# Performance work log

Measured on AMD Instinct MI355X. Metric: run time of the kernel, lower is better.

## Reference

```python
import jax, jax.numpy as jnp
import numpy as np

EPS_SCALE = 1e-4

def setup_inputs() -> dict:
    key = jax.random.key(0)
    B, D, K = 4096, 64, 256
    x = jax.random.normal(key, (B, D, K), dtype=jnp.float32)
    return {"x": x}

def reference(x):
    # x: [B, D, K]  (batch, cluster_dim, num_clusters) -- training path
    B, D, K = x.shape
    mu = jnp.mean(x, axis=0, keepdims=True)              # [1, D, K]
    xc = jnp.transpose(x - mu, (2, 1, 0))                # [K, D, B]
    cov = jnp.einsum('kdb,keb->kde', xc, xc) / (B - 1)   # [K, D, D]
    eps = EPS_SCALE * jnp.eye(D, dtype=x.dtype)
    L = jnp.linalg.cholesky(cov + eps)                   # [K, D, D]
    Z = jax.scipy.linalg.solve_triangular(L, xc, lower=True)  # [K, D, B]
    return jnp.transpose(Z, (2, 1, 0))                   # [B, D, K]
```

## Files before the change

### kernel.cpp

```cpp
#include <hip/hip_runtime.h>
#include <math.h>

#define Bn 4096
#define Dn 64
#define Kn 256
#define DKn 16384
#define SLAB ((size_t)262144)

typedef __attribute__((ext_vector_type(8))) short bf16x8;
typedef __attribute__((ext_vector_type(4))) float f32x4;
typedef unsigned short u16;
typedef unsigned int u32;

__device__ __forceinline__ float bf2f(u16 u) {
  return __uint_as_float(((u32)u) << 16);
}
__device__ __forceinline__ u16 f2bf(float f) {
  u32 x = __float_as_uint(f);
  u32 r = x + 0x7fffu + ((x >> 16) & 1u);
  return (u16)(r >> 16);
}

__global__ __launch_bounds__(256) void k1_transpose(
    const float* __restrict__ x, u16* __restrict__ xh) {
  __shared__ __align__(16) u16 tile[64][72];
  const int b0 = blockIdx.x * 8;
  const int k0 = blockIdx.y * 64;
  const int t = threadIdx.x;
  const int kq = t & 15, dsub = t >> 4;
  const int kr = t >> 3, dq = t & 7;

  for (int bb = 0; bb < 8; ++bb) {
    const int b = b0 + bb;
#pragma unroll
    for (int i = 0; i < 4; ++i) {
      const int d = dsub + 16 * i;
      const float4 v = *(const float4*)&x[(size_t)b * DKn + (size_t)d * Kn + k0 + 4 * kq];
      tile[4 * kq + 0][d] = f2bf(v.x);
      tile[4 * kq + 1][d] = f2bf(v.y);
      tile[4 * kq + 2][d] = f2bf(v.z);
      tile[4 * kq + 3][d] = f2bf(v.w);
    }
    __syncthreads();
#pragma unroll
    for (int it = 0; it < 2; ++it) {
      const int k = kr + 32 * it;
      const uint4 wv = *(const uint4*)&tile[k][8 * dq];
      *(uint4*)&xh[(size_t)(k0 + k) * SLAB + (size_t)b * 64 + 8 * dq] = wv;
    }
    __syncthreads();
  }
}

__global__ __launch_bounds__(256) void k2_cov(
    const u16* __restrict__ xh, float* __restrict__ covp, float* __restrict__ Sp) {
  __shared__ __align__(16) u16 tile[64][136];
  __shared__ float sred[32][64];
  const int part = blockIdx.x;
  const int k = blockIdx.y;
  const int t = threadIdx.x;
  const int w = t >> 6, l = t & 63;
  const int r16 = l & 15, g = l >> 4;
  const int dw = t & 7, bq = t >> 3;
  const u16* pk = xh + (size_t)k * SLAB;

  f32x4 hh[10];
#pragma unroll
  for (int p = 0; p < 10; ++p) hh[p] = (f32x4){0.f, 0.f, 0.f, 0.f};
  float sums[8];
#pragma unroll
  for (int jj = 0; jj < 8; ++jj) sums[jj] = 0.f;

  for (int sub = 0; sub < 8; ++sub) {
    const int bbase = part * 1024 + sub * 128;
    __syncthreads();
#pragma unroll
    for (int i = 0; i < 4; ++i) {
      const int b = bq * 4 + i;
      const uint4 v = *(const uint4*)&pk[(size_t)(bbase + b) * 64 + dw * 8];
      const u16* pv = (const u16*)&v;
#pragma unroll
      for (int jj = 0; jj < 8; ++jj) {
        const u16 h = pv[jj];
        sums[jj] += bf2f(h);
        tile[dw * 8 + jj][b] = h;
      }
    }
    __syncthreads();
    bf16x8 fr[4];
#pragma unroll
    for (int m = 0; m < 4; ++m)
      fr[m] = *(const bf16x8*)&tile[16 * m + r16][32 * w + 8 * g];
#pragma unroll
    for (int m = 0; m < 4; ++m)
#pragma unroll
      for (int n = m; n < 4; ++n) {
        const int p = (m * (7 - m)) / 2 + n;
        hh[p] = __builtin_amdgcn_mfma_f32_16x16x32_bf16(fr[m], fr[n], hh[p], 0, 0, 0);
      }
  }
  float* cp = covp + ((size_t)k * 16 + part * 4 + w) * 2560;
#pragma unroll
  for (int p = 0; p < 10; ++p)
#pragma unroll
    for (int r = 0; r < 4; ++r)
      cp[p * 256 + (g * 4 + r) * 16 + r16] = hh[p][r];
#pragma unroll
  for (int jj = 0; jj < 8; ++jj) sred[bq][dw * 8 + jj] = sums[jj];
  __syncthreads();
  if (t < 64) {
    float s = 0.f;
#pragma unroll
    for (int q = 0; q < 32; ++q) s += sred[q][t];
    Sp[((size_t)k * 4 + part) * 64 + t] = s;
  }
}

__global__ __launch_bounds__(256) void k3_chol(
    const float* __restrict__ covp, const float* __restrict__ Sp,
    u16* __restrict__ wt, u16* __restrict__ vout) {
  __shared__ float a[64][65];
  __shared__ float mus[64];
  __shared__ float colv[64];
  __shared__ float diag;
  const int k = blockIdx.x;
  const int tid = threadIdx.x;
  if (tid < 64) {
    float s = 0.f;
#pragma unroll
    for (int q = 0; q < 4; ++q) s += Sp[((size_t)k * 4 + q) * 64 + tid];
    mus[tid] = s * (1.f / 4096.f);
  }
  __syncthreads();
  const float* cp = covp + (size_t)k * 16 * 2560;
  for (int idx = tid; idx < 4096; idx += 256) {
    const int i = idx >> 6, j = idx & 63;
    const int i16 = i >> 4, j16 = j >> 4, r = i & 15, c = j & 15;
    int p, off;
    if (i16 <= j16) { p = (i16 * (7 - i16)) / 2 + j16; off = r * 16 + c; }
    else            { p = (j16 * (7 - j16)) / 2 + i16; off = c * 16 + r; }
    float s = 0.f;
#pragma unroll
    for (int q = 0; q < 16; ++q) s += cp[q * 2560 + p * 256 + off];
    float cv = (s - 4096.f * mus[i] * mus[j]) * (1.f / 4095.f);
    if (i == j) cv += 1e-4f;
    a[i][j] = cv;
  }
  __syncthreads();
  for (int j = 0; j < 64; ++j) {
    if (tid == j) diag = sqrtf(a[j][j]);
    __syncthreads();
    const float ljj = diag;
    float lij = 0.f;
    if (tid == j) a[j][j] = ljj;
    if (tid < 64 && tid > j) {
      lij = a[tid][j] / ljj;
      a[tid][j] = lij;
      colv[tid] = lij;
    }
    __syncthreads();
    if (tid < 64 && tid > j)
      for (int e = j + 1; e <= tid; ++e) a[tid][e] -= lij * colv[e];
    __syncthreads();
  }
  float wv[64];
  if (tid < 64) {
#pragma unroll
    for (int i = 0; i < 64; ++i) {
      float s2 = (i == tid) ? 1.f : 0.f;
#pragma unroll
      for (int j = 0; j < i; ++j) s2 -= a[i][j] * wv[j];
      wv[i] = (i >= tid) ? s2 / a[i][i] : 0.f;
    }
  }
  __syncthreads();
  if (tid < 64) {
#pragma unroll
    for (int i = 0; i < 64; ++i) a[i][tid] = wv[i];
  }
  __syncthreads();
  if (tid < 64) {
    float v = 0.f;
#pragma unroll
    for (int e = 0; e < 64; ++e) v += a[tid][e] * mus[e];
    vout[(size_t)k * 64 + tid] = f2bf(v);
  }
#pragma unroll
  for (int it = 0; it < 8; ++it) {
    const int idx = it * 256 + tid;
    const int dd = idx >> 5, ep = idx & 31;
    const u32 pk2 = (u32)f2bf(a[dd][2 * ep]) | ((u32)f2bf(a[dd][2 * ep + 1]) << 16);
    *(u32*)&wt[(size_t)k * 4096 + 2 * idx] = pk2;
  }
}

__global__ __launch_bounds__(256) void k45_solve(
    const u16* __restrict__ xh, const u16* __restrict__ wt,
    const u16* __restrict__ vin, float* __restrict__ out) {
  __shared__ __align__(16) u16 xstage[2][16][64];
  __shared__ u16 zb[64][16][34];
  __shared__ __align__(16) u16 vsh[32][64];
  const int b0 = blockIdx.x * 16;
  const int kc0 = blockIdx.y * 32;
  const int t = threadIdx.x;
  const int w = t >> 6, l = t & 63;
  const int r16 = l & 15, g = l >> 4;
  const int skl = t >> 7, sb = (t & 127) >> 3, sdq = t & 7;

  {
    const uint4 vv = *(const uint4*)&vin[(size_t)kc0 * 64 + t * 8];
    *(uint4*)&((u16*)vsh)[t * 8] = vv;
  }

  bf16x8 ac00, ac01, ac10, ac11, an00, an01, an10, an11;
  uint4 scur, snext;
  {
    const int k = kc0 + skl;
    scur = *(const uint4*)&xh[(size_t)k * SLAB + (size_t)(b0 + sb) * 64 + sdq * 8];
    const u16* wk0 = wt + (size_t)kc0 * 4096 + (16 * w + r16) * 64 + 8 * g;
    ac00 = *(const bf16x8*)(wk0);
    ac01 = *(const bf16x8*)(wk0 + 32);
    const u16* wk1 = wk0 + 4096;
    ac10 = *(const bf16x8*)(wk1);
    ac11 = *(const bf16x8*)(wk1 + 32);
  }

  for (int rnd = 0; rnd < 16; ++rnd) {
    if (rnd + 1 < 16) {
      const int k = kc0 + (rnd + 1) * 2 + skl;
      snext = *(const uint4*)&xh[(size_t)k * SLAB + (size_t)(b0 + sb) * 64 + sdq * 8];
      const u16* wk0 = wt + (size_t)(kc0 + (rnd + 1) * 2) * 4096 + (16 * w + r16) * 64 + 8 * g;
      an00 = *(const bf16x8*)(wk0);
      an01 = *(const bf16x8*)(wk0 + 32);
      const u16* wk1 = wk0 + 4096;
      an10 = *(const bf16x8*)(wk1);
      an11 = *(const bf16x8*)(wk1 + 32);
    }
    *(uint4*)&xstage[skl][sb][sdq * 8] = scur;
    __syncthreads();
#pragma unroll
    for (int kl = 0; kl < 2; ++kl) {
      const int k = rnd * 2 + kl;
      const bf16x8 bf0 = *(const bf16x8*)&xstage[kl][r16][8 * g];
      const bf16x8 bf1 = *(const bf16x8*)&xstage[kl][r16][32 + 8 * g];
      f32x4 acc = (f32x4){0.f, 0.f, 0.f, 0.f};
      if (kl == 0) {
        acc = __builtin_amdgcn_mfma_f32_16x16x32_bf16(ac00, bf0, acc, 0, 0, 0);
        acc = __builtin_amdgcn_mfma_f32_16x16x32_bf16(ac01, bf1, acc, 0, 0, 0);
      } else {
        acc = __builtin_amdgcn_mfma_f32_16x16x32_bf16(ac10, bf0, acc, 0, 0, 0);
        acc = __builtin_amdgcn_mfma_f32_16x16x32_bf16(ac11, bf1, acc, 0, 0, 0);
      }
#pragma unroll
      for (int r = 0; r < 4; ++r)
        zb[16 * w + 4 * g + r][r16][k] = f2bf(acc[r]);
    }
    scur = snext;
    ac00 = an00; ac01 = an01; ac10 = an10; ac11 = an11;
    __syncthreads();
  }

#pragma unroll
  for (int it = 0; it < 4; ++it) {
    const int b = 4 * w + it;
    const int d = l;
    float* op = &out[(size_t)(b0 + b) * DKn + (size_t)d * Kn + kc0];
#pragma unroll
    for (int q = 0; q < 8; ++q) {
      float4 ov;
      ov.x = bf2f(zb[d][b][4 * q + 0]) - bf2f(vsh[4 * q + 0][d]);
      ov.y = bf2f(zb[d][b][4 * q + 1]) - bf2f(vsh[4 * q + 1][d]);
      ov.z = bf2f(zb[d][b][4 * q + 2]) - bf2f(vsh[4 * q + 2][d]);
      ov.w = bf2f(zb[d][b][4 * q + 3]) - bf2f(vsh[4 * q + 3][d]);
      *(float4*)&op[4 * q] = ov;
    }
  }
}

extern "C" void kernel_launch(void* const* d_in, const int* in_sizes, int n_in,
                              void* d_out, int out_size, void* d_ws, size_t ws_size,
                              hipStream_t stream) {
  (void)in_sizes; (void)n_in; (void)out_size;
  const float* x = (const float*)d_in[0];
  float* out = (float*)d_out;
  char* ws = (char*)d_ws;
  const size_t XH_B = 134217728;
  const size_t CP_B = 41943040;
  const size_t SP_B = 262144;
  const size_t WT_B = 2097152;
  const size_t V_B  = 32768;
  if (ws_size < XH_B + CP_B + SP_B + WT_B + V_B) return;
  u16* xh = (u16*)ws;
  float* covp = (float*)(ws + XH_B);
  float* Sp = (float*)(ws + XH_B + CP_B);
  u16* wtb = (u16*)(ws + XH_B + CP_B + SP_B);
  u16* vb  = (u16*)(ws + XH_B + CP_B + SP_B + WT_B);

  k1_transpose<<<dim3(512, 4), 256, 0, stream>>>(x, xh);
  k2_cov<<<dim3(4, 256), 256, 0, stream>>>(xh, covp, Sp);
  k3_chol<<<dim3(256), 256, 0, stream>>>(covp, Sp, wtb, vb);
  k45_solve<<<dim3(256, 8), 256, 0, stream>>>(xh, wtb, vb, out);
}
```

Baseline: 376.8 us.

## Stage eight clusters per round with XOR-swizzled LDS and register-held results

Restructures the solve kernel to load x tiles for eight clusters per round into double-buffered, XOR-swizzled shared memory. This cuts the number of barriers from 32 to about 4 and avoids LDS bank conflicts on the MFMA operand reads. Results are now packed as bf16 in 64 registers per thread instead of going through a large shared zb buffer, and the output is written directly from those registers. This lowers LDS traffic and use, but raises register pressure, which may reduce occupancy or cause spills.

```diff
diff --git a/kernel.cpp b/kernel.cpp
--- a/kernel.cpp
+++ b/kernel.cpp
@@ -197,81 +197,94 @@
 __global__ __launch_bounds__(256) void k45_solve(
     const u16* __restrict__ xh, const u16* __restrict__ wt,
     const u16* __restrict__ vin, float* __restrict__ out) {
-  __shared__ __align__(16) u16 xstage[2][16][64];
-  __shared__ u16 zb[64][16][34];
+  __shared__ __align__(16) u16 xstage[2][8][16][64];
   __shared__ __align__(16) u16 vsh[32][64];
   const int b0 = blockIdx.x * 16;
   const int kc0 = blockIdx.y * 32;
   const int t = threadIdx.x;
   const int w = t >> 6, l = t & 63;
   const int r16 = l & 15, g = l >> 4;
-  const int skl = t >> 7, sb = (t & 127) >> 3, sdq = t & 7;
-
+
+  *(uint4*)&((u16*)vsh)[t * 8] = *(const uint4*)&vin[(size_t)kc0 * 64 + t * 8];
+
+  uint4 sv[4];
+#pragma unroll
+  for (int i = 0; i < 4; ++i) {
+    const int idx = i * 256 + t;
+    const int kk = idx >> 7, b = (idx >> 3) & 15, dc = idx & 7;
+    sv[i] = *(const uint4*)&xh[(size_t)(kc0 + kk) * SLAB + (size_t)(b0 + b) * 64 + dc * 8];
+  }
+#pragma unroll
+  for (int i = 0; i < 4; ++i) {
+    const int idx = i * 256 + t;
+    const int kk = idx >> 7, b = (idx >> 3) & 15, dc = idx & 7;
+    *(uint4*)&xstage[0][kk][b][(dc ^ (b & 7)) * 8] = sv[i];
+  }
+  __syncthreads();
+
+  bf16x8 a0, a1, an0, an1;
   {
-    const uint4 vv = *(const uint4*)&vin[(size_t)kc0 * 64 + t * 8];
-    *(uint4*)&((u16*)vsh)[t * 8] = vv;
-  }
-
-  bf16x8 ac00, ac01, ac10, ac11, an00, an01, an10, an11;
-  uint4 scur, snext;
-  {
-    const int k = kc0 + skl;
-    scur = *(const uint4*)&xh[(size_t)k * SLAB + (size_t)(b0 + sb) * 64 + sdq * 8];
-    const u16* wk0 = wt + (size_t)kc0 * 4096 + (16 * w + r16) * 64 + 8 * g;
-    ac00 = *(const bf16x8*)(wk0);
-    ac01 = *(const bf16x8*)(wk0 + 32);
-    const u16* wk1 = wk0 + 4096;
-    ac10 = *(const bf16x8*)(wk1);
-    ac11 = *(const bf16x8*)(wk1 + 32);
-  }
-
-  for (int rnd = 0; rnd < 16; ++rnd) {
-    if (rnd + 1 < 16) {
-      const int k = kc0 + (rnd + 1) * 2 + skl;
-      snext = *(const uint4*)&xh[(size_t)k * SLAB + (size_t)(b0 + sb) * 64 + sdq * 8];
-      const u16* wk0 = wt + (size_t)(kc0 + (rnd + 1) * 2) * 4096 + (16 * w + r16) * 64 + 8 * g;
-      an00 = *(const bf16x8*)(wk0);
-      an01 = *(const bf16x8*)(wk0 + 32);
-      const u16* wk1 = wk0 + 4096;
-      an10 = *(const bf16x8*)(wk1);
-      an11 = *(const bf16x8*)(wk1 + 32);
-    }
-    *(uint4*)&xstage[skl][sb][sdq * 8] = scur;
-    __syncthreads();
-#pragma unroll
-    for (int kl = 0; kl < 2; ++kl) {
-      const int k = rnd * 2 + kl;
-      const bf16x8 bf0 = *(const bf16x8*)&xstage[kl][r16][8 * g];
-      const bf16x8 bf1 = *(const bf16x8*)&xstage[kl][r16][32 + 8 * g];
+    const u16* wk = wt + (size_t)kc0 * 4096 + (16 * w + r16) * 64 + 8 * g;
+    a0 = *(const bf16x8*)(wk);
+    a1 = *(const bf16x8*)(wk + 32);
+  }
+
+  u32 zr[64];
+
+#pragma unroll
+  for (int rnd = 0; rnd < 4; ++rnd) {
+    if (rnd < 3) {
+#pragma unroll
+      for (int i = 0; i < 4; ++i) {
+        const int idx = i * 256 + t;
+        const int kk = idx >> 7, b = (idx >> 3) & 15, dc = idx & 7;
+        sv[i] = *(const uint4*)&xh[(size_t)(kc0 + (rnd + 1) * 8 + kk) * SLAB +
+                                   (size_t)(b0 + b) * 64 + dc * 8];
+      }
+    }
+#pragma unroll
+    for (int kk = 0; kk < 8; ++kk) {
+      const int kidx = rnd * 8 + kk;
+      if (kidx < 31) {
+        const u16* wk = wt + (size_t)(kc0 + kidx + 1) * 4096 + (16 * w + r16) * 64 + 8 * g;
+        an0 = *(const bf16x8*)(wk);
+        an1 = *(const bf16x8*)(wk + 32);
+      }
+      const bf16x8 bf0 = *(const bf16x8*)&xstage[rnd & 1][kk][r16][(g ^ (r16 & 7)) * 8];
+      const bf16x8 bf1 = *(const bf16x8*)&xstage[rnd & 1][kk][r16][((4 + g) ^ (r16 & 7)) * 8];
       f32x4 acc = (f32x4){0.f, 0.f, 0.f, 0.f};
-      if (kl == 0) {
-        acc = __builtin_amdgcn_mfma_f32_16x16x32_bf16(ac00, bf0, acc, 0, 0, 0);
-        acc = __builtin_amdgcn_mfma_f32_16x16x32_bf16(ac01, bf1, acc, 0, 0, 0);
-      } else {
-        acc = __builtin_amdgcn_mfma_f32_16x16x32_bf16(ac10, bf0, acc, 0, 0, 0);
-        acc = __builtin_amdgcn_mfma_f32_16x16x32_bf16(ac11, bf1, acc, 0, 0, 0);
-      }
-#pragma unroll
-      for (int r = 0; r < 4; ++r)
-        zb[16 * w + 4 * g + r][r16][k] = f2bf(acc[r]);
-    }
-    scur = snext;
-    ac00 = an00; ac01 = an01; ac10 = an10; ac11 = an11;
-    __syncthreads();
-  }
-
-#pragma unroll
-  for (int it = 0; it < 4; ++it) {
-    const int b = 4 * w + it;
-    const int d = l;
-    float* op = &out[(size_t)(b0 + b) * DKn + (size_t)d * Kn + kc0];
+      acc = __builtin_amdgcn_mfma_f32_16x16x32_bf16(a0, bf0, acc, 0, 0, 0);
+      acc = __builtin_amdgcn_mfma_f32_16x16x32_bf16(a1, bf1, acc, 0, 0, 0);
+      zr[2 * kidx] = (u32)f2bf(acc[0]) | ((u32)f2bf(acc[1]) << 16);
+      zr[2 * kidx + 1] = (u32)f2bf(acc[2]) | ((u32)f2bf(acc[3]) << 16);
+      a0 = an0; a1 = an1;
+    }
+    if (rnd < 3) {
+#pragma unroll
+      for (int i = 0; i < 4; ++i) {
+        const int idx = i * 256 + t;
+        const int kk = idx >> 7, b = (idx >> 3) & 15, dc = idx & 7;
+        *(uint4*)&xstage[(rnd + 1) & 1][kk][b][(dc ^ (b & 7)) * 8] = sv[i];
+      }
+      __syncthreads();
+    }
+  }
+
+#pragma unroll
+  for (int r = 0; r < 4; ++r) {
+    const int d = 16 * w + 4 * g + r;
+    float* op = &out[(size_t)(b0 + r16) * DKn + (size_t)d * Kn + kc0];
 #pragma unroll
     for (int q = 0; q < 8; ++q) {
       float4 ov;
-      ov.x = bf2f(zb[d][b][4 * q + 0]) - bf2f(vsh[4 * q + 0][d]);
-      ov.y = bf2f(zb[d][b][4 * q + 1]) - bf2f(vsh[4 * q + 1][d]);
-      ov.z = bf2f(zb[d][b][4 * q + 2]) - bf2f(vsh[4 * q + 2][d]);
-      ov.w = bf2f(zb[d][b][4 * q + 3]) - bf2f(vsh[4 * q + 3][d]);
+#pragma unroll
+      for (int s = 0; s < 4; ++s) {
+        const int k = 4 * q + s;
+        const u32 word = zr[2 * k + (r >> 1)];
+        const float z = (r & 1) ? __uint_as_float(word & 0xffff0000u)
+                                : __uint_as_float(word << 16);
+        ((float*)&ov)[s] = z - bf2f(vsh[k][d]);
+      }
       *(float4*)&op[4 * q] = ov;
     }
   }
```

New measurement: 504.4 us. 1.34x slower.
